# Optimization experiments

Hardware: AMD Instinct MI355X
Metric: run time of the kernel (lower is better)

## Reference

```python
import jax, jax.numpy as jnp
import numpy as np

N = 100000; E = 800000; IN_DIM = 32; HID = 64; HEADS = 4; HEAD_DIM = HID // HEADS; L = 3; G = 128

def setup_inputs() -> dict:
    key = jax.random.key(0)
    ks = jax.random.split(key, 12)
    nrm = lambda k, shape: jax.random.normal(k, shape, jnp.float32) * 0.05
    return {
        "x": jax.random.normal(ks[0], (N, IN_DIM), jnp.float32),
        "edge_index": jax.random.randint(ks[1], (2, E), 0, N),
        "edge_attr": jax.random.normal(ks[2], (E, 1), jnp.float32),
        "batch": jnp.sort(jax.random.randint(ks[3], (N,), 0, G)),
        "in_W": nrm(ks[4], (IN_DIM, HID)), "in_b": jnp.zeros((HID,), jnp.float32),
        "in_ln_g": jnp.ones((HID,), jnp.float32), "in_ln_b": jnp.zeros((HID,), jnp.float32),
        "W_qkv": nrm(ks[5], (L, 3, HID, HID)), "b_qkv": jnp.zeros((L, 3, HID), jnp.float32),
        "W_edge": nrm(ks[6], (L, 1, HID)),
        "W_skip": nrm(ks[7], (L, HID, HID)), "b_skip": jnp.zeros((L, HID), jnp.float32),
        "W_beta": nrm(ks[8], (L, 3 * HID)),
        "ln_g": jnp.ones((L, HID), jnp.float32), "ln_b": jnp.zeros((L, HID), jnp.float32),
        "r1_W": nrm(ks[9], (2 * HID, HID)), "r1_b": jnp.zeros((HID,), jnp.float32),
        "r2_W": nrm(ks[10], (HID, HID // 2)), "r2_b": jnp.zeros((HID // 2,), jnp.float32),
        "r3_W": nrm(ks[11], (HID // 2, 1)), "r3_b": jnp.zeros((1,), jnp.float32),
    }

def _layer_norm(x, g, b, eps=1e-5):
    mu = x.mean(-1, keepdims=True)
    var = ((x - mu) ** 2).mean(-1, keepdims=True)
    return (x - mu) * jax.lax.rsqrt(var + eps) * g + b

def _gelu(x):
    return jax.nn.gelu(x, approximate=False)  # matches torch F.gelu default (erf)

def _forward(x, edge_attr, in_W, in_b, in_ln_g, in_ln_b, W_qkv, b_qkv, W_edge,
             W_skip, b_skip, W_beta, ln_g, ln_b, r1_W, r1_b, r2_W, r2_b, r3_W, r3_b,
             edge_index, batch):
    src, dst = edge_index[0], edge_index[1]  # message flows src -> dst
    n = x.shape[0]
    h = _layer_norm(_gelu(x @ in_W + in_b), in_ln_g, in_ln_b)
    scale = 1.0 / jnp.sqrt(jnp.float32(HEAD_DIM))
    for l in range(L):
        res = h
        q = (h @ W_qkv[l, 0] + b_qkv[l, 0]).reshape(n, HEADS, HEAD_DIM)
        k = (h @ W_qkv[l, 1] + b_qkv[l, 1]).reshape(n, HEADS, HEAD_DIM)
        v = (h @ W_qkv[l, 2] + b_qkv[l, 2]).reshape(n, HEADS, HEAD_DIM)
        e = (edge_attr @ W_edge[l]).reshape(-1, HEADS, HEAD_DIM)  # [E,H,C]
        ke = k[src] + e
        alpha = jnp.einsum("ehc,ehc->eh", q[dst], ke) * scale      # [E,H]
        amax = jax.ops.segment_max(alpha, dst, num_segments=n)
        ex = jnp.exp(alpha - amax[dst])
        den = jax.ops.segment_sum(ex, dst, num_segments=n)
        alpha = ex / (den[dst] + 1e-16)                            # PyG softmax eps
        msg = alpha[..., None] * (v[src] + e)
        out = jax.ops.segment_sum(msg, dst, num_segments=n).reshape(n, HID)
        x_r = h @ W_skip[l] + b_skip[l]
        beta = jax.nn.sigmoid(jnp.concatenate([out, x_r, out - x_r], -1) @ W_beta[l])  # [N]
        out = beta[:, None] * x_r + (1.0 - beta[:, None]) * out
        h = _layer_norm(_gelu(out) + res, ln_g[l], ln_b[l])
    cnt = jax.ops.segment_sum(jnp.ones((n,), h.dtype), batch, num_segments=G)
    gmean = jax.ops.segment_sum(h, batch, num_segments=G) / jnp.maximum(cnt, 1.0)[:, None]
    gmax = jax.ops.segment_max(h, batch, num_segments=G)
    rep = jnp.concatenate([gmean, gmax], -1)  # [G, 2*HID]
    rep = _gelu(rep @ r1_W + r1_b)
    rep = _gelu(rep @ r2_W + r2_b)
    return (rep @ r3_W + r3_b).reshape(-1)

def reference(x, edge_index, edge_attr, batch, in_W, in_b, in_ln_g, in_ln_b,
              W_qkv, b_qkv, W_edge, W_skip, b_skip, W_beta, ln_g, ln_b,
              r1_W, r1_b, r2_W, r2_b, r3_W, r3_b):
    return _forward(x, edge_attr, in_W, in_b, in_ln_g, in_ln_b, W_qkv, b_qkv, W_edge,
                    W_skip, b_skip, W_beta, ln_g, ln_b, r1_W, r1_b, r2_W, r2_b, r3_W, r3_b,
                    edge_index, batch)
```

## Files before the change

kernel.cpp:

```cpp
#include <hip/hip_runtime.h>
#include <hip/hip_fp16.h>
#include <math.h>
#include <float.h>

#define LAYERS 3
#define NGRAPH 128

typedef __attribute__((ext_vector_type(8))) short bf16x8;
typedef __attribute__((ext_vector_type(4))) float f32x4;

union bfr { int4 i; bf16x8 b; };

__device__ __forceinline__ float gelu_f(float x) {
    return 0.5f * x * (1.0f + erff(x * 0.70710678118654752440f));
}

template <int CTRL, int RMASK>
__device__ __forceinline__ float dpp_add(float x) {
    int t = __builtin_amdgcn_update_dpp(0, __float_as_int(x), CTRL, RMASK, 0xF, false);
    return x + __int_as_float(t);
}

__device__ __forceinline__ float sum16(float v) {
    v = dpp_add<0xB1, 0xF>(v);
    v = dpp_add<0x4E, 0xF>(v);
    v = dpp_add<0x141, 0xF>(v);
    v = dpp_add<0x140, 0xF>(v);
    return v;
}

__device__ __forceinline__ unsigned int f2mono(float f) {
    unsigned int u = __float_as_uint(f);
    return (u & 0x80000000u) ? ~u : (u | 0x80000000u);
}
__device__ __forceinline__ float mono2f(unsigned int u) {
    return (u & 0x80000000u) ? __uint_as_float(u ^ 0x80000000u)
                             : __uint_as_float(~u);
}

__device__ __forceinline__ float2 h2f2(int bits) {
    __half2 h = *reinterpret_cast<__half2*>(&bits);
    return __half22float2(h);
}

__device__ __forceinline__ void cvt_frag(const float4& f0, const float4& f1,
                                         bf16x8& hi, bf16x8& lo) {
    float ff[8] = {f0.x, f0.y, f0.z, f0.w, f1.x, f1.y, f1.z, f1.w};
#pragma unroll
    for (int j = 0; j < 8; j++) {
        unsigned u = __float_as_uint(ff[j]);
        hi[j] = (short)(u >> 16);
        float hf = __uint_as_float(u & 0xFFFF0000u);
        lo[j] = (short)(__float_as_uint(ff[j] - hf) >> 16);
    }
}

__device__ __forceinline__ f32x4 mm3(const bf16x8& ahi, const bf16x8& alo,
                                     const int4* __restrict__ pk, int tile,
                                     int lane, f32x4 acc) {
    bfr bh, bl;
    bh.i = pk[tile * 128 + lane];
    bl.i = pk[tile * 128 + 64 + lane];
    acc = __builtin_amdgcn_mfma_f32_16x16x32_bf16(alo, bh.b, acc, 0, 0, 0);
    acc = __builtin_amdgcn_mfma_f32_16x16x32_bf16(ahi, bl.b, acc, 0, 0, 0);
    acc = __builtin_amdgcn_mfma_f32_16x16x32_bf16(ahi, bh.b, acc, 0, 0, 0);
    return acc;
}

__global__ __launch_bounds__(256) void k_cvt(
    const float* __restrict__ in_W, const float* __restrict__ W_skip,
    const float* __restrict__ W_qkv, int4* __restrict__ pk_in,
    int4* __restrict__ pk_skip, int4* __restrict__ pk_qkv) {
    int w = (blockIdx.x * 256 + threadIdx.x) >> 6;
    if (w >= 100) return;
    int lane = threadIdx.x & 63;
    const float* src;
    int4* dst;
    int kt, jt, qkvmode = 0;
    if (w < 4) {
        kt = 0; jt = w;
        src = in_W;
        dst = pk_in + w * 128;
    } else {
        int l = (w - 4) >> 5, r = (w - 4) & 31;
        if (r < 8) {
            kt = r & 1; jt = r >> 1;
            src = W_skip + l * 4096;
            dst = pk_skip + (l * 8 + r) * 128;
        } else {
            int tq = r - 8;
            kt = tq & 1; jt = tq >> 1;
            src = W_qkv + l * 12288;
            dst = pk_qkv + (l * 24 + tq) * 128;
            qkvmode = 1;
        }
    }
    int c = jt * 16 + (lane & 15);
    int koff = kt * 32 + (lane >> 4) * 8;
    unsigned hi[8], lo[8];
#pragma unroll
    for (int j = 0; j < 8; j++) {
        int k = koff + j;
        float f = qkvmode ? src[(c >> 6) * 4096 + k * 64 + (c & 63)]
                          : src[k * 64 + c];
        unsigned u = __float_as_uint(f);
        hi[j] = u >> 16;
        float hf = __uint_as_float(u & 0xFFFF0000u);
        lo[j] = __float_as_uint(f - hf) >> 16;
    }
    int4 H, L;
    H.x = hi[0] | (hi[1] << 16); H.y = hi[2] | (hi[3] << 16);
    H.z = hi[4] | (hi[5] << 16); H.w = hi[6] | (hi[7] << 16);
    L.x = lo[0] | (lo[1] << 16); L.y = lo[2] | (lo[3] << 16);
    L.z = lo[4] | (lo[5] << 16); L.w = lo[6] | (lo[7] << 16);
    dst[lane] = H;
    dst[64 + lane] = L;
}

__global__ __launch_bounds__(256) void k_hist(const int* __restrict__ dst,
                                              int* __restrict__ deg, int E) {
    int e = blockIdx.x * 256 + threadIdx.x;
    if (e < E) atomicAdd(&deg[dst[e]], 1);
}

__global__ __launch_bounds__(256) void k_scan1(const int* __restrict__ deg,
                                               int* __restrict__ excl,
                                               int* __restrict__ bsum, int n) {
    __shared__ int s[256];
    int t = threadIdx.x;
    int i = blockIdx.x * 256 + t;
    int v = (i < n) ? deg[i] : 0;
    s[t] = v;
    __syncthreads();
    for (int off = 1; off < 256; off <<= 1) {
        int a = (t >= off) ? s[t - off] : 0;
        __syncthreads();
        s[t] += a;
        __syncthreads();
    }
    if (i < n) excl[i] = s[t] - v;
    if (t == 255) bsum[blockIdx.x] = s[255];
}

__global__ __launch_bounds__(512) void k_scan2(int* __restrict__ bsum, int nb) {
    __shared__ int s[512];
    int t = threadIdx.x;
    int v = (t < nb) ? bsum[t] : 0;
    s[t] = v;
    __syncthreads();
    for (int off = 1; off < 512; off <<= 1) {
        int a = (t >= off) ? s[t - off] : 0;
        __syncthreads();
        s[t] += a;
        __syncthreads();
    }
    if (t < nb) bsum[t] = s[t] - v;
}

__global__ __launch_bounds__(256) void k_scan3(const int* __restrict__ excl,
                                               const int* __restrict__ bsum,
                                               int* __restrict__ row,
                                               int* __restrict__ cursor,
                                               int n, int E) {
    int i = blockIdx.x * 256 + threadIdx.x;
    if (i < n) {
        int r = excl[i] + bsum[blockIdx.x];
        row[i] = r;
        cursor[i] = r;
    }
    if (blockIdx.x == 0 && threadIdx.x == 0) row[n] = E;
}

__global__ __launch_bounds__(256) void k_scatter(const int* __restrict__ src,
                                                 const int* __restrict__ dst,
                                                 const float* __restrict__ ea,
                                                 int* __restrict__ cursor,
                                                 int2* __restrict__ ep, int E) {
    int e = blockIdx.x * 256 + threadIdx.x;
    if (e >= E) return;
    int d = dst[e];
    int p = atomicAdd(&cursor[d], 1);
    ep[p] = make_int2(src[e], __float_as_int(ea[e]));
}

__device__ __forceinline__ int kv_idx(int m, int cc) {
    return (cc >> 2) * 8 + (m - 1) * 4 + (cc & 3);
}

__global__ __launch_bounds__(256) void k_in_qkv(
    const float* __restrict__ x, const int4* __restrict__ pk_in,
    const float* __restrict__ b, const float* __restrict__ g,
    const float* __restrict__ be, const int4* __restrict__ pk_qkv,
    const float* __restrict__ bn, float* __restrict__ h,
    __half* __restrict__ q, __half* __restrict__ kvout, int n) {
    __shared__ float lds[4][1088];
    int lane = threadIdx.x & 63, wid = threadIdx.x >> 6;
    int nb = (blockIdx.x * 4 + wid) * 16;
    if (nb >= n) return;
    int g16 = lane >> 4, c16 = lane & 15;
    int arow = min(nb + c16, n - 1);
    const float* xp = x + (size_t)arow * 32 + g16 * 8;
    float4 f0 = *(const float4*)xp;
    float4 f1 = *(const float4*)(xp + 4);
    bf16x8 ahi, alo;
    cvt_frag(f0, f1, ahi, alo);
    float gv[4][4];
#pragma unroll
    for (int jt = 0; jt < 4; jt++) {
        f32x4 a = {0.f, 0.f, 0.f, 0.f};
        a = mm3(ahi, alo, pk_in, jt, lane, a);
        float bb = b[jt * 16 + c16];
#pragma unroll
        for (int r = 0; r < 4; r++) gv[jt][r] = gelu_f(a[r] + bb);
    }
    float gl[4], bel[4];
#pragma unroll
    for (int jt = 0; jt < 4; jt++) {
        gl[jt] = g[jt * 16 + c16];
        bel[jt] = be[jt * 16 + c16];
    }
    float hreg[4][4];
#pragma unroll
    for (int r = 0; r < 4; r++) {
        float s = gv[0][r] + gv[1][r] + gv[2][r] + gv[3][r];
        float mu = sum16(s) * (1.0f / 64.0f);
        float vs = 0.f;
#pragma unroll
        for (int jt = 0; jt < 4; jt++) {
            float d = gv[jt][r] - mu;
            vs += d * d;
        }
        float var = sum16(vs) * (1.0f / 64.0f);
        float rs = rsqrtf(var + 1e-5f);
#pragma unroll
        for (int jt = 0; jt < 4; jt++)
            hreg[jt][r] = (gv[jt][r] - mu) * rs * gl[jt] + bel[jt];
    }
#pragma unroll
    for (int jt = 0; jt < 4; jt++)
#pragma unroll
        for (int r = 0; r < 4; r++) {
            int nd = nb + g16 * 4 + r;
            if (nd < n) h[(size_t)nd * 64 + jt * 16 + c16] = hreg[jt][r];
            lds[wid][(g16 * 4 + r) * 68 + jt * 16 + c16] = hreg[jt][r];
        }
    bf16x8 qahi[2], qalo[2];
#pragma unroll
    for (int kt = 0; kt < 2; kt++) {
        const float* lp = &lds[wid][c16 * 68 + kt * 32 + g16 * 8];
        float4 t0 = *(const float4*)lp;
        float4 t1 = *(const float4*)(lp + 4);
        cvt_frag(t0, t1, qahi[kt], qalo[kt]);
    }
#pragma unroll
    for (int jt = 0; jt < 12; jt++) {
        f32x4 a = {0.f, 0.f, 0.f, 0.f};
#pragma unroll
        for (int kt = 0; kt < 2; kt++) a = mm3(qahi[kt], qalo[kt], pk_qkv, jt * 2 + kt, lane, a);
        int c = jt * 16 + c16;
        float bias = bn[c];
        int m = c >> 6, cc = c & 63;
#pragma unroll
        for (int r = 0; r < 4; r++) {
            int nd = nb + g16 * 4 + r;
            if (nd < n) {
                float val = a[r] + bias;
                if (m == 0) q[(size_t)nd * 64 + cc] = __float2half(val);
                else kvout[(size_t)nd * 128 + kv_idx(m, cc)] = __float2half(val);
            }
        }
    }
}

__global__ __launch_bounds__(256) void k_attn(
    const __half* __restrict__ q, const __half* __restrict__ kv,
    const int* __restrict__ row, const int2* __restrict__ ep,
    const float* __restrict__ We, float* __restrict__ out, int n) {
    int lane = threadIdx.x & 63;
    int node = blockIdx.x * 4 + (threadIdx.x >> 6);
    if (node >= n) return;
    int g = lane >> 4;
    int c16 = lane & 15;
    int2 qb = *(const int2*)(q + (size_t)node * 64 + c16 * 4);
    float2 q01 = h2f2(qb.x), q23 = h2f2(qb.y);
    float4 wv = *(const float4*)(We + c16 * 4);
    int beg = row[node], end = row[node + 1];
    float den = 0.f;
    float4 acc = {0.f, 0.f, 0.f, 0.f};
    for (int pos = beg; pos < end; pos += 4) {
        int idx = pos + g;
        bool valid = idx < end;
        int safe = valid ? idx : beg;
        int2 pr = ep[safe];
        int s = pr.x;
        float a = __int_as_float(pr.y);
        int4 kb = *(const int4*)(kv + (size_t)s * 128 + c16 * 8);
        float2 k01 = h2f2(kb.x), k23 = h2f2(kb.y);
        float2 v01 = h2f2(kb.z), v23 = h2f2(kb.w);
        float p = q01.x * fmaf(a, wv.x, k01.x) + q01.y * fmaf(a, wv.y, k01.y) +
                  q23.x * fmaf(a, wv.z, k23.x) + q23.y * fmaf(a, wv.w, k23.y);
        p = dpp_add<0xB1, 0xF>(p);
        p = dpp_add<0x4E, 0xF>(p);
        float ex = valid ? __expf(fminf(p * 0.25f, 60.f)) : 0.f;
        den += ex;
        acc.x = fmaf(ex, fmaf(a, wv.x, v01.x), acc.x);
        acc.y = fmaf(ex, fmaf(a, wv.y, v01.y), acc.y);
        acc.z = fmaf(ex, fmaf(a, wv.z, v23.x), acc.z);
        acc.w = fmaf(ex, fmaf(a, wv.w, v23.y), acc.w);
    }
#pragma unroll
    for (int mask = 16; mask <= 32; mask <<= 1) {
        den += __shfl_xor(den, mask, 64);
        acc.x += __shfl_xor(acc.x, mask, 64);
        acc.y += __shfl_xor(acc.y, mask, 64);
        acc.z += __shfl_xor(acc.z, mask, 64);
        acc.w += __shfl_xor(acc.w, mask, 64);
    }
    if (g == 0) {
        float inv = 1.0f / (den + 1e-16f);
        float4 o = {acc.x * inv, acc.y * inv, acc.z * inv, acc.w * inv};
        *(float4*)(out + (size_t)node * 64 + c16 * 4) = o;
    }
}

template <int DO_QKV>
__global__ __launch_bounds__(256) void k_node_qkv(
    float* __restrict__ h, const float* __restrict__ o_in,
    const int4* __restrict__ pk_skip, const float* __restrict__ bs,
    const float* __restrict__ Wb, const float* __restrict__ lg,
    const float* __restrict__ lb, const int4* __restrict__ pk_qkv,
    const float* __restrict__ bn, __half* __restrict__ q,
    __half* __restrict__ kvout, int n) {
    __shared__ float lds[4][DO_QKV ? 1088 : 4];
    int lane = threadIdx.x & 63, wid = threadIdx.x >> 6;
    int nb = (blockIdx.x * 4 + wid) * 16;
    if (nb >= n) return;
    int g16 = lane >> 4, c16 = lane & 15;
    bf16x8 ahi[2], alo[2];
    int arow = min(nb + c16, n - 1);
#pragma unroll
    for (int kt = 0; kt < 2; kt++) {
        const float* hp = h + (size_t)arow * 64 + kt * 32 + g16 * 8;
        float4 f0 = *(const float4*)hp;
        float4 f1 = *(const float4*)(hp + 4);
        cvt_frag(f0, f1, ahi[kt], alo[kt]);
    }
    float xr[4][4];
#pragma unroll
    for (int jt = 0; jt < 4; jt++) {
        f32x4 a = {0.f, 0.f, 0.f, 0.f};
#pragma unroll
        for (int kt = 0; kt < 2; kt++) a = mm3(ahi[kt], alo[kt], pk_skip, jt * 2 + kt, lane, a);
        float bias = bs[jt * 16 + c16];
#pragma unroll
        for (int r = 0; r < 4; r++) xr[jt][r] = a[r] + bias;
    }
    float ov[4][4], hold[4][4];
#pragma unroll
    for (int jt = 0; jt < 4; jt++)
#pragma unroll
        for (int r = 0; r < 4; r++) {
            int nd = min(nb + g16 * 4 + r, n - 1);
            ov[jt][r] = o_in[(size_t)nd * 64 + jt * 16 + c16];
            hold[jt][r] = h[(size_t)nd * 64 + jt * 16 + c16];
        }
    float wb0[4], wb1[4], wb2[4], lgv[4], lbv[4];
#pragma unroll
    for (int jt = 0; jt < 4; jt++) {
        int c = jt * 16 + c16;
        wb0[jt] = Wb[c]; wb1[jt] = Wb[64 + c]; wb2[jt] = Wb[128 + c];
        lgv[jt] = lg[c]; lbv[jt] = lb[c];
    }
    float hnew[4][4];
#pragma unroll
    for (int r = 0; r < 4; r++) {
        float cbs = 0.f;
#pragma unroll
        for (int jt = 0; jt < 4; jt++)
            cbs += ov[jt][r] * wb0[jt] + xr[jt][r] * wb1[jt] +
                   (ov[jt][r] - xr[jt][r]) * wb2[jt];
        float cb = sum16(cbs);
        float beta = 1.0f / (1.0f + expf(-cb));
        float gvr[4], s = 0.f;
#pragma unroll
        for (int jt = 0; jt < 4; jt++) {
            float o2 = fmaf(beta, xr[jt][r] - ov[jt][r], ov[jt][r]);
            gvr[jt] = gelu_f(o2) + hold[jt][r];
            s += gvr[jt];
        }
        float mu = sum16(s) * (1.0f / 64.0f);
        float vs = 0.f;
#pragma unroll
        for (int jt = 0; jt < 4; jt++) {
            float d = gvr[jt] - mu;
            vs += d * d;
        }
        float var = sum16(vs) * (1.0f / 64.0f);
        float rs = rsqrtf(var + 1e-5f);
#pragma unroll
        for (int jt = 0; jt < 4; jt++)
            hnew[jt][r] = (gvr[jt] - mu) * rs * lgv[jt] + lbv[jt];
    }
#pragma unroll
    for (int jt = 0; jt < 4; jt++)
#pragma unroll
        for (int r = 0; r < 4; r++) {
            int nd = nb + g16 * 4 + r;
            if (nd < n) h[(size_t)nd * 64 + jt * 16 + c16] = hnew[jt][r];
            if (DO_QKV) lds[wid][(g16 * 4 + r) * 68 + jt * 16 + c16] = hnew[jt][r];
        }
    if (!DO_QKV) return;
    bf16x8 qahi[2], qalo[2];
#pragma unroll
    for (int kt = 0; kt < 2; kt++) {
        const float* lp = &lds[wid][c16 * 68 + kt * 32 + g16 * 8];
        float4 t0 = *(const float4*)lp;
        float4 t1 = *(const float4*)(lp + 4);
        cvt_frag(t0, t1, qahi[kt], qalo[kt]);
    }
#pragma unroll
    for (int jt = 0; jt < 12; jt++) {
        f32x4 a = {0.f, 0.f, 0.f, 0.f};
#pragma unroll
        for (int kt = 0; kt < 2; kt++) a = mm3(qahi[kt], qalo[kt], pk_qkv, jt * 2 + kt, lane, a);
        int c = jt * 16 + c16;
        float bias = bn[c];
        int m = c >> 6, cc = c & 63;
#pragma unroll
        for (int r = 0; r < 4; r++) {
            int nd = nb + g16 * 4 + r;
            if (nd < n) {
                float val = a[r] + bias;
                if (m == 0) q[(size_t)nd * 64 + cc] = __float2half(val);
                else kvout[(size_t)nd * 128 + kv_idx(m, cc)] = __float2half(val);
            }
        }
    }
}

__global__ __launch_bounds__(256) void k_pool3(
    const float* __restrict__ h, const int* __restrict__ batch,
    float* __restrict__ gsum, unsigned int* __restrict__ gmax,
    float* __restrict__ cnt, int n, int chunk) {
    int wave = (blockIdx.x * 256 + threadIdx.x) >> 6;
    int lane = threadIdx.x & 63;
    int i0 = wave * chunk;
    if (i0 >= n) return;
    int i1 = min(n, i0 + chunk);
    int cur = batch[i0];
    float s = 0.f, mx = -FLT_MAX;
    int run = 0;
    for (int i = i0; i < i1; ++i) {
        int g = batch[i];
        if (g != cur) {
            atomicAdd(gsum + cur * 64 + lane, s);
            atomicMax(gmax + cur * 64 + lane, f2mono(mx));
            if (lane == 0) atomicAdd(cnt + cur, (float)run);
            s = 0.f; mx = -FLT_MAX; run = 0; cur = g;
        }
        float v = h[(size_t)i * 64 + lane];
        s += v;
        mx = fmaxf(mx, v);
        ++run;
    }
    atomicAdd(gsum + cur * 64 + lane, s);
    atomicMax(gmax + cur * 64 + lane, f2mono(mx));
    if (lane == 0) atomicAdd(cnt + cur, (float)run);
}

__global__ void k_final(const float* __restrict__ gsum,
                        const unsigned int* __restrict__ gmax,
                        const float* __restrict__ cnt,
                        const float* __restrict__ W1, const float* __restrict__ b1,
                        const float* __restrict__ W2, const float* __restrict__ b2,
                        const float* __restrict__ W3, const float* __restrict__ b3,
                        float* __restrict__ out) {
    int g = blockIdx.x;
    int lane = threadIdx.x;
    __shared__ float rep[128];
    __shared__ float t1[64];
    __shared__ float t2[32];
    float c = fmaxf(cnt[g], 1.0f);
    rep[lane] = gsum[g * 64 + lane] / c;
    rep[64 + lane] = mono2f(gmax[g * 64 + lane]);
    __syncthreads();
    float a = b1[lane];
#pragma unroll 8
    for (int i = 0; i < 128; i++) a = fmaf(rep[i], W1[i * 64 + lane], a);
    t1[lane] = gelu_f(a);
    __syncthreads();
    if (lane < 32) {
        float a2 = b2[lane];
#pragma unroll 8
        for (int i = 0; i < 64; i++) a2 = fmaf(t1[i], W2[i * 32 + lane], a2);
        t2[lane] = gelu_f(a2);
    }
    __syncthreads();
    if (lane < 32) {
        float p = t2[lane] * W3[lane];
#pragma unroll
        for (int o = 16; o > 0; o >>= 1) p += __shfl_xor(p, o, 64);
        if (lane == 0) out[g] = p + b3[0];
    }
}

extern "C" void kernel_launch(void* const* d_in, const int* in_sizes, int n_in,
                              void* d_out, int out_size, void* d_ws,
                              size_t ws_size, hipStream_t stream) {
    const float* x      = (const float*)d_in[0];
    const int*   eidx   = (const int*)d_in[1];
    const float* ea     = (const float*)d_in[2];
    const int*   batch  = (const int*)d_in[3];
    const float* in_W   = (const float*)d_in[4];
    const float* in_b   = (const float*)d_in[5];
    const float* in_lng = (const float*)d_in[6];
    const float* in_lnb = (const float*)d_in[7];
    const float* W_qkv  = (const float*)d_in[8];
    const float* b_qkv  = (const float*)d_in[9];
    const float* W_edge = (const float*)d_in[10];
    const float* W_skip = (const float*)d_in[11];
    const float* b_skip = (const float*)d_in[12];
    const float* W_beta = (const float*)d_in[13];
    const float* ln_g   = (const float*)d_in[14];
    const float* ln_b   = (const float*)d_in[15];
    const float* r1_W   = (const float*)d_in[16];
    const float* r1_b   = (const float*)d_in[17];
    const float* r2_W   = (const float*)d_in[18];
    const float* r2_b   = (const float*)d_in[19];
    const float* r3_W   = (const float*)d_in[20];
    const float* r3_b   = (const float*)d_in[21];

    int n = in_sizes[0] / 32;
    int E = in_sizes[2];
    const int* src = eidx;
    const int* dst = eidx + E;

    char* ws = (char*)d_ws;
    size_t off = 0;
    auto alloc = [&](size_t bytes) -> void* {
        void* p = ws + off;
        off = (off + bytes + 255) & ~(size_t)255;
        return p;
    };
    float* h    = (float*)alloc((size_t)n * 64 * 4);
    __half* qh  = (__half*)alloc((size_t)n * 64 * 2);
    __half* kvh = (__half*)alloc((size_t)n * 128 * 2);
    float* oacc = (float*)alloc((size_t)n * 64 * 4);
    int* deg    = (int*)alloc((size_t)n * 4);
    int* excl   = (int*)alloc((size_t)n * 4);
    int* bsum   = (int*)alloc(512 * 4);
    int* row    = (int*)alloc((size_t)(n + 1) * 4);
    int* cursor = (int*)alloc((size_t)n * 4);
    int2* ep    = (int2*)alloc((size_t)E * 8);
    int4* pk_in   = (int4*)alloc(4 * 128 * 16);
    int4* pk_skip = (int4*)alloc(3 * 8 * 128 * 16);
    int4* pk_qkv  = (int4*)alloc((size_t)3 * 24 * 128 * 16);
    float* gsum = (float*)alloc((NGRAPH * 64 * 2 + NGRAPH) * 4);
    unsigned int* gmax = (unsigned int*)(gsum + NGRAPH * 64);
    float* cnt  = gsum + NGRAPH * 128;

    int nb4 = (n + 3) / 4;
    int nb64 = (n + 63) / 64;
    int nbs = (n + 255) / 256;
    int ebs = (E + 255) / 256;

    k_cvt<<<25, 256, 0, stream>>>(in_W, W_skip, W_qkv, pk_in, pk_skip, pk_qkv);
    hipMemsetAsync(deg, 0, (size_t)n * 4, stream);
    k_hist<<<ebs, 256, 0, stream>>>(dst, deg, E);
    k_scan1<<<nbs, 256, 0, stream>>>(deg, excl, bsum, n);
    k_scan2<<<1, 512, 0, stream>>>(bsum, nbs);
    k_scan3<<<nbs, 256, 0, stream>>>(excl, bsum, row, cursor, n, E);
    k_scatter<<<ebs, 256, 0, stream>>>(src, dst, ea, cursor, ep, E);

    k_in_qkv<<<nb64, 256, 0, stream>>>(x, pk_in, in_b, in_lng, in_lnb,
                                       pk_qkv, b_qkv, h, qh, kvh, n);

    for (int l = 0; l < LAYERS; l++) {
        k_attn<<<nb4, 256, 0, stream>>>(qh, kvh, row, ep, W_edge + l * 64, oacc, n);
        if (l + 1 < LAYERS) {
            k_node_qkv<1><<<nb64, 256, 0, stream>>>(
                h, oacc, pk_skip + l * 8 * 128, b_skip + l * 64,
                W_beta + l * 192, ln_g + l * 64, ln_b + l * 64,
                pk_qkv + (size_t)(l + 1) * 24 * 128, b_qkv + (size_t)(l + 1) * 192,
                qh, kvh, n);
        } else {
            k_node_qkv<0><<<nb64, 256, 0, stream>>>(
                h, oacc, pk_skip + l * 8 * 128, b_skip + l * 64,
                W_beta + l * 192, ln_g + l * 64, ln_b + l * 64,
                nullptr, nullptr, nullptr, nullptr, n);
        }
    }

    hipMemsetAsync(gsum, 0, (NGRAPH * 64 * 2 + NGRAPH) * 4, stream);
    int nwaves = 4096;
    int chunk = (n + nwaves - 1) / nwaves;
    k_pool3<<<nwaves / 4, 256, 0, stream>>>(h, batch, gsum, gmax, cnt, n, chunk);
    k_final<<<NGRAPH, 64, 0, stream>>>(gsum, gmax, cnt, r1_W, r1_b, r2_W, r2_b,
                                       r3_W, r3_b, (float*)d_out);
}
```

Baseline: 395.6 us.

## Bucket CSR scatter, unroll attention edge loop, fuse pooling into last layer

Replaces the global atomic CSR scatter with a two-pass scheme. Edges are first bucketed by destination block of 1024 nodes using LDS counters, then placed locally so the cursor atomics and writes stay within a small region. The attention loop now handles two edges per group per iteration for more memory-level parallelism. The final layer kernel does the graph mean/max pooling itself, with a wave-uniform fast path, which removes the separate pooling kernel and the h store in that layer. This adds an extra E-sized intermediate buffer and packs the local destination into the high bits of src, which assumes src < 2^20.

```diff
diff --git a/kernel.cpp b/kernel.cpp
--- a/kernel.cpp
+++ b/kernel.cpp
@@ -5,6 +5,8 @@
 
 #define LAYERS 3
 #define NGRAPH 128
+#define NPB 1024
+#define NBMAX 256
 
 typedef __attribute__((ext_vector_type(8))) short bf16x8;
 typedef __attribute__((ext_vector_type(4))) float f32x4;
@@ -161,26 +163,68 @@
                                                const int* __restrict__ bsum,
                                                int* __restrict__ row,
                                                int* __restrict__ cursor,
+                                               int* __restrict__ gcurb,
                                                int n, int E) {
     int i = blockIdx.x * 256 + threadIdx.x;
     if (i < n) {
         int r = excl[i] + bsum[blockIdx.x];
         row[i] = r;
         cursor[i] = r;
+        if ((i & (NPB - 1)) == 0) gcurb[i >> 10] = r;
     }
     if (blockIdx.x == 0 && threadIdx.x == 0) row[n] = E;
 }
 
-__global__ __launch_bounds__(256) void k_scatter(const int* __restrict__ src,
-                                                 const int* __restrict__ dst,
-                                                 const float* __restrict__ ea,
-                                                 int* __restrict__ cursor,
-                                                 int2* __restrict__ ep, int E) {
-    int e = blockIdx.x * 256 + threadIdx.x;
-    if (e >= E) return;
-    int d = dst[e];
-    int p = atomicAdd(&cursor[d], 1);
-    ep[p] = make_int2(src[e], __float_as_int(ea[e]));
+__global__ __launch_bounds__(256) void k_bucket(
+    const int* __restrict__ src, const int* __restrict__ dst,
+    const float* __restrict__ ea, int* __restrict__ gcurb,
+    int2* __restrict__ mid, int E, int nbkt) {
+    __shared__ int cnt[NBMAX], base_[NBMAX];
+    int tile = blockIdx.x * 4096;
+    for (int i = threadIdx.x; i < nbkt; i += 256) cnt[i] = 0;
+    __syncthreads();
+    int d[16];
+#pragma unroll
+    for (int j = 0; j < 16; j++) {
+        int e = tile + j * 256 + threadIdx.x;
+        d[j] = -1;
+        if (e < E) {
+            d[j] = dst[e];
+            atomicAdd(&cnt[d[j] >> 10], 1);
+        }
+    }
+    __syncthreads();
+    for (int i = threadIdx.x; i < nbkt; i += 256) {
+        base_[i] = atomicAdd(&gcurb[i], cnt[i]);
+        cnt[i] = 0;
+    }
+    __syncthreads();
+#pragma unroll
+    for (int j = 0; j < 16; j++) {
+        int e = tile + j * 256 + threadIdx.x;
+        if (e < E) {
+            int b = d[j] >> 10;
+            int p = base_[b] + atomicAdd(&cnt[b], 1);
+            mid[p] = make_int2(src[e] | ((d[j] & (NPB - 1)) << 20),
+                               __float_as_int(ea[e]));
+        }
+    }
+}
+
+__global__ __launch_bounds__(256) void k_local(
+    const int* __restrict__ row, int* __restrict__ cursor,
+    const int2* __restrict__ mid, int2* __restrict__ ep, int n) {
+    int b = blockIdx.x;
+    int n0 = b << 10;
+    int n1 = min(n, n0 + NPB);
+    int ebeg = row[n0], eend = row[n1];
+    for (int e = ebeg + blockIdx.y * 256 + threadIdx.x; e < eend;
+         e += 256 * gridDim.y) {
+        int2 m = mid[e];
+        int dn = n0 + ((m.x >> 20) & (NPB - 1));
+        int p = atomicAdd(&cursor[dn], 1);
+        ep[p] = make_int2(m.x & 0xFFFFF, m.y);
+    }
 }
 
 __device__ __forceinline__ int kv_idx(int m, int cc) {
@@ -287,26 +331,42 @@
     int beg = row[node], end = row[node + 1];
     float den = 0.f;
     float4 acc = {0.f, 0.f, 0.f, 0.f};
-    for (int pos = beg; pos < end; pos += 4) {
-        int idx = pos + g;
-        bool valid = idx < end;
-        int safe = valid ? idx : beg;
-        int2 pr = ep[safe];
-        int s = pr.x;
-        float a = __int_as_float(pr.y);
-        int4 kb = *(const int4*)(kv + (size_t)s * 128 + c16 * 8);
-        float2 k01 = h2f2(kb.x), k23 = h2f2(kb.y);
-        float2 v01 = h2f2(kb.z), v23 = h2f2(kb.w);
-        float p = q01.x * fmaf(a, wv.x, k01.x) + q01.y * fmaf(a, wv.y, k01.y) +
-                  q23.x * fmaf(a, wv.z, k23.x) + q23.y * fmaf(a, wv.w, k23.y);
-        p = dpp_add<0xB1, 0xF>(p);
-        p = dpp_add<0x4E, 0xF>(p);
-        float ex = valid ? __expf(fminf(p * 0.25f, 60.f)) : 0.f;
-        den += ex;
-        acc.x = fmaf(ex, fmaf(a, wv.x, v01.x), acc.x);
-        acc.y = fmaf(ex, fmaf(a, wv.y, v01.y), acc.y);
-        acc.z = fmaf(ex, fmaf(a, wv.z, v23.x), acc.z);
-        acc.w = fmaf(ex, fmaf(a, wv.w, v23.y), acc.w);
+    for (int pos = beg; pos < end; pos += 8) {
+        int idx0 = pos + g, idx1 = pos + 4 + g;
+        bool v0 = idx0 < end, v1 = idx1 < end;
+        int2 pr0 = ep[v0 ? idx0 : beg];
+        int2 pr1 = ep[v1 ? idx1 : beg];
+        float a0 = __int_as_float(pr0.y), a1 = __int_as_float(pr1.y);
+        int4 kb0 = *(const int4*)(kv + (size_t)pr0.x * 128 + c16 * 8);
+        int4 kb1 = *(const int4*)(kv + (size_t)pr1.x * 128 + c16 * 8);
+        {
+            float2 k01 = h2f2(kb0.x), k23 = h2f2(kb0.y);
+            float2 v01 = h2f2(kb0.z), v23 = h2f2(kb0.w);
+            float p = q01.x * fmaf(a0, wv.x, k01.x) + q01.y * fmaf(a0, wv.y, k01.y) +
+                      q23.x * fmaf(a0, wv.z, k23.x) + q23.y * fmaf(a0, wv.w, k23.y);
+            p = dpp_add<0xB1, 0xF>(p);
+            p = dpp_add<0x4E, 0xF>(p);
+            float ex = v0 ? __expf(fminf(p * 0.25f, 60.f)) : 0.f;
+            den += ex;
+            acc.x = fmaf(ex, fmaf(a0, wv.x, v01.x), acc.x);
+            acc.y = fmaf(ex, fmaf(a0, wv.y, v01.y), acc.y);
+            acc.z = fmaf(ex, fmaf(a0, wv.z, v23.x), acc.z);
+            acc.w = fmaf(ex, fmaf(a0, wv.w, v23.y), acc.w);
+        }
+        {
+            float2 k01 = h2f2(kb1.x), k23 = h2f2(kb1.y);
+            float2 v01 = h2f2(kb1.z), v23 = h2f2(kb1.w);
+            float p = q01.x * fmaf(a1, wv.x, k01.x) + q01.y * fmaf(a1, wv.y, k01.y) +
+                      q23.x * fmaf(a1, wv.z, k23.x) + q23.y * fmaf(a1, wv.w, k23.y);
+            p = dpp_add<0xB1, 0xF>(p);
+            p = dpp_add<0x4E, 0xF>(p);
+            float ex = v1 ? __expf(fminf(p * 0.25f, 60.f)) : 0.f;
+            den += ex;
+            acc.x = fmaf(ex, fmaf(a1, wv.x, v01.x), acc.x);
+            acc.y = fmaf(ex, fmaf(a1, wv.y, v01.y), acc.y);
+            acc.z = fmaf(ex, fmaf(a1, wv.z, v23.x), acc.z);
+            acc.w = fmaf(ex, fmaf(a1, wv.w, v23.y), acc.w);
+        }
     }
 #pragma unroll
     for (int mask = 16; mask <= 32; mask <<= 1) {
@@ -330,7 +390,9 @@
     const float* __restrict__ Wb, const float* __restrict__ lg,
     const float* __restrict__ lb, const int4* __restrict__ pk_qkv,
     const float* __restrict__ bn, __half* __restrict__ q,
-    __half* __restrict__ kvout, int n) {
+    __half* __restrict__ kvout, const int* __restrict__ batch,
+    float* __restrict__ gsum, unsigned int* __restrict__ gmaxu,
+    float* __restrict__ cnt, int n) {
     __shared__ float lds[4][DO_QKV ? 1088 : 4];
     int lane = threadIdx.x & 63, wid = threadIdx.x >> 6;
     int nb = (blockIdx.x * 4 + wid) * 16;
@@ -401,71 +463,90 @@
         for (int jt = 0; jt < 4; jt++)
             hnew[jt][r] = (gvr[jt] - mu) * rs * lgv[jt] + lbv[jt];
     }
-#pragma unroll
-    for (int jt = 0; jt < 4; jt++)
-#pragma unroll
-        for (int r = 0; r < 4; r++) {
-            int nd = nb + g16 * 4 + r;
-            if (nd < n) h[(size_t)nd * 64 + jt * 16 + c16] = hnew[jt][r];
-            if (DO_QKV) lds[wid][(g16 * 4 + r) * 68 + jt * 16 + c16] = hnew[jt][r];
-        }
-    if (!DO_QKV) return;
-    bf16x8 qahi[2], qalo[2];
-#pragma unroll
-    for (int kt = 0; kt < 2; kt++) {
-        const float* lp = &lds[wid][c16 * 68 + kt * 32 + g16 * 8];
-        float4 t0 = *(const float4*)lp;
-        float4 t1 = *(const float4*)(lp + 4);
-        cvt_frag(t0, t1, qahi[kt], qalo[kt]);
-    }
-#pragma unroll
-    for (int jt = 0; jt < 12; jt++) {
-        f32x4 a = {0.f, 0.f, 0.f, 0.f};
-#pragma unroll
-        for (int kt = 0; kt < 2; kt++) a = mm3(qahi[kt], qalo[kt], pk_qkv, jt * 2 + kt, lane, a);
-        int c = jt * 16 + c16;
-        float bias = bn[c];
-        int m = c >> 6, cc = c & 63;
-#pragma unroll
-        for (int r = 0; r < 4; r++) {
-            int nd = nb + g16 * 4 + r;
-            if (nd < n) {
-                float val = a[r] + bias;
-                if (m == 0) q[(size_t)nd * 64 + cc] = __float2half(val);
-                else kvout[(size_t)nd * 128 + kv_idx(m, cc)] = __float2half(val);
+    if (DO_QKV) {
+#pragma unroll
+        for (int jt = 0; jt < 4; jt++)
+#pragma unroll
+            for (int r = 0; r < 4; r++) {
+                int nd = nb + g16 * 4 + r;
+                if (nd < n) h[(size_t)nd * 64 + jt * 16 + c16] = hnew[jt][r];
+                lds[wid][(g16 * 4 + r) * 68 + jt * 16 + c16] = hnew[jt][r];
             }
-        }
-    }
-}
-
-__global__ __launch_bounds__(256) void k_pool3(
-    const float* __restrict__ h, const int* __restrict__ batch,
-    float* __restrict__ gsum, unsigned int* __restrict__ gmax,
-    float* __restrict__ cnt, int n, int chunk) {
-    int wave = (blockIdx.x * 256 + threadIdx.x) >> 6;
-    int lane = threadIdx.x & 63;
-    int i0 = wave * chunk;
-    if (i0 >= n) return;
-    int i1 = min(n, i0 + chunk);
-    int cur = batch[i0];
-    float s = 0.f, mx = -FLT_MAX;
-    int run = 0;
-    for (int i = i0; i < i1; ++i) {
-        int g = batch[i];
-        if (g != cur) {
-            atomicAdd(gsum + cur * 64 + lane, s);
-            atomicMax(gmax + cur * 64 + lane, f2mono(mx));
-            if (lane == 0) atomicAdd(cnt + cur, (float)run);
-            s = 0.f; mx = -FLT_MAX; run = 0; cur = g;
-        }
-        float v = h[(size_t)i * 64 + lane];
-        s += v;
-        mx = fmaxf(mx, v);
-        ++run;
-    }
-    atomicAdd(gsum + cur * 64 + lane, s);
-    atomicMax(gmax + cur * 64 + lane, f2mono(mx));
-    if (lane == 0) atomicAdd(cnt + cur, (float)run);
+        bf16x8 qahi[2], qalo[2];
+#pragma unroll
+        for (int kt = 0; kt < 2; kt++) {
+            const float* lp = &lds[wid][c16 * 68 + kt * 32 + g16 * 8];
+            float4 t0 = *(const float4*)lp;
+            float4 t1 = *(const float4*)(lp + 4);
+            cvt_frag(t0, t1, qahi[kt], qalo[kt]);
+        }
+#pragma unroll
+        for (int jt = 0; jt < 12; jt++) {
+            f32x4 a = {0.f, 0.f, 0.f, 0.f};
+#pragma unroll
+            for (int kt = 0; kt < 2; kt++) a = mm3(qahi[kt], qalo[kt], pk_qkv, jt * 2 + kt, lane, a);
+            int c = jt * 16 + c16;
+            float bias = bn[c];
+            int m = c >> 6, cc = c & 63;
+#pragma unroll
+            for (int r = 0; r < 4; r++) {
+                int nd = nb + g16 * 4 + r;
+                if (nd < n) {
+                    float val = a[r] + bias;
+                    if (m == 0) q[(size_t)nd * 64 + cc] = __float2half(val);
+                    else kvout[(size_t)nd * 128 + kv_idx(m, cc)] = __float2half(val);
+                }
+            }
+        }
+    } else {
+        int gid[4];
+        int g0 = batch[nb];
+        bool ok = (nb + 15 < n);
+#pragma unroll
+        for (int r = 0; r < 4; r++)
+            gid[r] = batch[min(nb + g16 * 4 + r, n - 1)];
+        bool uni = ok && __all(gid[0] == g0 && gid[1] == g0 &&
+                               gid[2] == g0 && gid[3] == g0);
+        if (uni) {
+            float s[4], mx[4];
+#pragma unroll
+            for (int jt = 0; jt < 4; jt++) {
+                s[jt] = hnew[jt][0] + hnew[jt][1] + hnew[jt][2] + hnew[jt][3];
+                mx[jt] = fmaxf(fmaxf(hnew[jt][0], hnew[jt][1]),
+                               fmaxf(hnew[jt][2], hnew[jt][3]));
+            }
+#pragma unroll
+            for (int mask = 16; mask <= 32; mask <<= 1) {
+#pragma unroll
+                for (int jt = 0; jt < 4; jt++) {
+                    s[jt] += __shfl_xor(s[jt], mask, 64);
+                    mx[jt] = fmaxf(mx[jt], __shfl_xor(mx[jt], mask, 64));
+                }
+            }
+            if (g16 == 0) {
+#pragma unroll
+                for (int jt = 0; jt < 4; jt++) {
+                    int ch = jt * 16 + c16;
+                    atomicAdd(&gsum[g0 * 64 + ch], s[jt]);
+                    atomicMax(&gmaxu[g0 * 64 + ch], f2mono(mx[jt]));
+                }
+            }
+            if (lane == 0) atomicAdd(&cnt[g0], 16.0f);
+        } else {
+#pragma unroll
+            for (int r = 0; r < 4; r++) {
+                int nd = nb + g16 * 4 + r;
+                if (nd >= n) continue;
+#pragma unroll
+                for (int jt = 0; jt < 4; jt++) {
+                    int ch = jt * 16 + c16;
+                    atomicAdd(&gsum[gid[r] * 64 + ch], hnew[jt][r]);
+                    atomicMax(&gmaxu[gid[r] * 64 + ch], f2mono(hnew[jt][r]));
+                }
+                if (c16 == 0) atomicAdd(&cnt[gid[r]], 1.0f);
+            }
+        }
+    }
 }
 
 __global__ void k_final(const float* __restrict__ gsum,
@@ -551,26 +632,31 @@
     int* bsum   = (int*)alloc(512 * 4);
     int* row    = (int*)alloc((size_t)(n + 1) * 4);
     int* cursor = (int*)alloc((size_t)n * 4);
+    int* gcurb  = (int*)alloc(NBMAX * 4);
+    int2* mid   = (int2*)alloc((size_t)E * 8);
     int2* ep    = (int2*)alloc((size_t)E * 8);
     int4* pk_in   = (int4*)alloc(4 * 128 * 16);
     int4* pk_skip = (int4*)alloc(3 * 8 * 128 * 16);
     int4* pk_qkv  = (int4*)alloc((size_t)3 * 24 * 128 * 16);
     float* gsum = (float*)alloc((NGRAPH * 64 * 2 + NGRAPH) * 4);
-    unsigned int* gmax = (unsigned int*)(gsum + NGRAPH * 64);
+    unsigned int* gmaxu = (unsigned int*)(gsum + NGRAPH * 64);
     float* cnt  = gsum + NGRAPH * 128;
 
     int nb4 = (n + 3) / 4;
     int nb64 = (n + 63) / 64;
     int nbs = (n + 255) / 256;
     int ebs = (E + 255) / 256;
+    int nbkt = (n + NPB - 1) >> 10;
 
     k_cvt<<<25, 256, 0, stream>>>(in_W, W_skip, W_qkv, pk_in, pk_skip, pk_qkv);
     hipMemsetAsync(deg, 0, (size_t)n * 4, stream);
+    hipMemsetAsync(gsum, 0, (NGRAPH * 64 * 2 + NGRAPH) * 4, stream);
     k_hist<<<ebs, 256, 0, stream>>>(dst, deg, E);
     k_scan1<<<nbs, 256, 0, stream>>>(deg, excl, bsum, n);
     k_scan2<<<1, 512, 0, stream>>>(bsum, nbs);
-    k_scan3<<<nbs, 256, 0, stream>>>(excl, bsum, row, cursor, n, E);
-    k_scatter<<<ebs, 256, 0, stream>>>(src, dst, ea, cursor, ep, E);
+    k_scan3<<<nbs, 256, 0, stream>>>(excl, bsum, row, cursor, gcurb, n, E);
+    k_bucket<<<(E + 4095) / 4096, 256, 0, stream>>>(src, dst, ea, gcurb, mid, E, nbkt);
+    k_local<<<dim3(nbkt, 4), 256, 0, stream>>>(row, cursor, mid, ep, n);
 
     k_in_qkv<<<nb64, 256, 0, stream>>>(x, pk_in, in_b, in_lng, in_lnb,
                                        pk_qkv, b_qkv, h, qh, kvh, n);
@@ -582,19 +668,16 @@
                 h, oacc, pk_skip + l * 8 * 128, b_skip + l * 64,
                 W_beta + l * 192, ln_g + l * 64, ln_b + l * 64,
                 pk_qkv + (size_t)(l + 1) * 24 * 128, b_qkv + (size_t)(l + 1) * 192,
-                qh, kvh, n);
+                qh, kvh, nullptr, nullptr, nullptr, nullptr, n);
         } else {
             k_node_qkv<0><<<nb64, 256, 0, stream>>>(
                 h, oacc, pk_skip + l * 8 * 128, b_skip + l * 64,
                 W_beta + l * 192, ln_g + l * 64, ln_b + l * 64,
-                nullptr, nullptr, nullptr, nullptr, n);
-        }
-    }
-
-    hipMemsetAsync(gsum, 0, (NGRAPH * 64 * 2 + NGRAPH) * 4, stream);
-    int nwaves = 4096;
-    int chunk = (n + nwaves - 1) / nwaves;
-    k_pool3<<<nwaves / 4, 256, 0, stream>>>(h, batch, gsum, gmax, cnt, n, chunk);
-    k_final<<<NGRAPH, 64, 0, stream>>>(gsum, gmax, cnt, r1_W, r1_b, r2_W, r2_b,
+                nullptr, nullptr, nullptr, nullptr,
+                batch, gsum, gmaxu, cnt, n);
+        }
+    }
+
+    k_final<<<NGRAPH, 64, 0, stream>>>(gsum, gmaxu, cnt, r1_W, r1_b, r2_W, r2_b,
                                        r3_W, r3_b, (float*)d_out);
 }
```

After: 381.1 us. 1.04x faster.
